# Performance work log

Measured on AMD Instinct MI355X. Metric: run time of the kernel, lower is better.

The kernel has to match this reference:

```python
import jax, jax.numpy as jnp
import numpy as np

# --- Instant-NGP hashgrid config (from INGP.build_encoding) ---
L = 16            # cfg_model.encoding.levels
F = 2             # cfg_model.encoding.hashgrid.dim
T = 1 << 19       # 2 ** log2_hashmap_size
BASE = 16         # 2 ** min_logres
FINEST = 2048     # 2 ** max_logres
GROWTH = np.exp((np.log(FINEST) - np.log(BASE)) / (L - 1))
RES = np.floor(BASE * GROWTH ** np.arange(L)).astype(np.float32)  # per-level resolution
VMIN, VMAX = -1.0, 1.0  # voxel_range
N_POINTS = 524288

# 8 trilinear corner offsets, and NGP spatial-hash primes
CORNERS = np.array([[i, j, k] for i in (0, 1) for j in (0, 1) for k in (0, 1)],
                   dtype=np.uint32)                       # [8,3]
PRIMES = np.array([1, 2654435761, 805459861], dtype=np.uint32)


def setup_inputs() -> dict:
    key = jax.random.key(0)
    k1, k2 = jax.random.split(key)
    points_3D = jax.random.uniform(k1, (N_POINTS, 3), minval=-1.0, maxval=1.0,
                                   dtype=jnp.float32)
    # torch-ngp 'uniform' init: U(-1e-4, 1e-4)
    tables = jax.random.uniform(k2, (L, T, F), minval=-1e-4, maxval=1e-4,
                                dtype=jnp.float32)
    return {"points_3D": points_3D, "tables": tables}


def _hash_encode(x, tables):
    """x: [N,3] in [0,1]; tables: [L,T,F] -> [N, L*F]."""
    corners_u = jnp.asarray(CORNERS)            # [8,3] uint32
    corners_b = jnp.asarray(CORNERS.astype(bool))
    p0u, p1u, p2u = (jnp.uint32(int(p)) for p in PRIMES)
    mask = jnp.uint32(T - 1)

    def level(table, r):
        pos = x * r                              # [N,3]
        p0 = jnp.floor(pos)
        w = pos - p0                             # trilinear weights [N,3]
        c = p0.astype(jnp.uint32)[:, None, :] + corners_u[None]  # [N,8,3]
        h = (c[..., 0] * p0u) ^ (c[..., 1] * p1u) ^ (c[..., 2] * p2u)
        idx = (h & mask).astype(jnp.int32)       # [N,8] hashed bucket ids
        vals = table[idx]                        # [N,8,F] irregular gather
        wc = jnp.where(corners_b[None], w[:, None, :], 1.0 - w[:, None, :]).prod(-1)
        return jnp.einsum('nc,ncf->nf', wc, vals)  # [N,F]

    feats = jax.vmap(level)(tables, jnp.asarray(RES))  # [L,N,F]
    n = x.shape[0]
    return jnp.transpose(feats, (1, 0, 2)).reshape(n, L * F)


def reference(points_3D, tables):
    # _encode_3D with contract=False: normalize to [0,1] over voxel_range
    x = (points_3D - VMIN) / (VMAX - VMIN)
    feat = _hash_encode(x, tables)
    return feat.astype(jnp.float32)
```

## Files before the change

kernel.cpp:

```cpp
#include <hip/hip_runtime.h>
#include <cmath>


constexpr int LVLS = 16;
constexpr unsigned TBL = 1u << 19;
constexpr unsigned TMASK = TBL - 1u;
constexpr unsigned P1 = 2654435761u;
constexpr unsigned P2 = 805459861u;
constexpr int PTS_PER_BLOCK = 512;
constexpr int NBINS = 32768;

typedef float vf2 __attribute__((ext_vector_type(2)));
typedef float vf4 __attribute__((ext_vector_type(4)));

struct ResArr { float r[LVLS]; };

__device__ __forceinline__ unsigned spread5(unsigned v) {
    v &= 31u;
    v = (v | (v << 8)) & 0x100Fu;
    v = (v | (v << 4)) & 0x10C3u;
    v = (v | (v << 2)) & 0x1249u;
    return v;
}

__device__ __forceinline__ unsigned bin_key(float px, float py, float pz) {
    float x = (px + 1.0f) * 0.5f;
    float y = (py + 1.0f) * 0.5f;
    float z = (pz + 1.0f) * 0.5f;
    unsigned bx = (unsigned)fminf(31.f, fmaxf(0.f, floorf(x * 32.f)));
    unsigned by = (unsigned)fminf(31.f, fmaxf(0.f, floorf(y * 32.f)));
    unsigned bz = (unsigned)fminf(31.f, fmaxf(0.f, floorf(z * 32.f)));
    return spread5(bx) | (spread5(by) << 1) | (spread5(bz) << 2);
}

__global__ __launch_bounds__(256) void ingp_hist(
    const float* __restrict__ pts, unsigned* __restrict__ hist, int npts)
{
    int i = blockIdx.x * 256 + threadIdx.x;
    if (i >= npts) return;
    float px = pts[i * 3 + 0], py = pts[i * 3 + 1], pz = pts[i * 3 + 2];
    atomicAdd(&hist[bin_key(px, py, pz)], 1u);
}

__global__ __launch_bounds__(1024) void ingp_scan(
    const unsigned* __restrict__ hist, unsigned* __restrict__ offs)
{
    __shared__ unsigned sc[1024];
    int t = threadIdx.x;
    unsigned loc[32];
    unsigned s = 0;
    #pragma unroll
    for (int i = 0; i < 32; ++i) { loc[i] = s; s += hist[t * 32 + i]; }
    sc[t] = s;
    __syncthreads();
    for (int d = 1; d < 1024; d <<= 1) {
        unsigned v = (t >= d) ? sc[t - d] : 0u;
        __syncthreads();
        sc[t] += v;
        __syncthreads();
    }
    unsigned base = sc[t] - s;
    #pragma unroll
    for (int i = 0; i < 32; ++i) offs[t * 32 + i] = base + loc[i];
}

__global__ __launch_bounds__(256) void ingp_scatter(
    const float* __restrict__ pts, unsigned* __restrict__ offs,
    vf4* __restrict__ pts4, int* __restrict__ perm, int npts)
{
    int i = blockIdx.x * 256 + threadIdx.x;
    if (i >= npts) return;
    float px = pts[i * 3 + 0], py = pts[i * 3 + 1], pz = pts[i * 3 + 2];
    unsigned pos = atomicAdd(&offs[bin_key(px, py, pz)], 1u);
    vf4 o; o.x = px; o.y = py; o.z = pz; o.w = __int_as_float(i);
    pts4[pos] = o;
    perm[pos] = i;
}

template<bool USE_WS, bool PACKED>
__global__ __launch_bounds__(256) void ingp_gather(
    const float* __restrict__ pts,
    const vf4* __restrict__ pts4,
    const float* __restrict__ tables,
    float2* __restrict__ dst,
    ResArr ra, int npts, int bpl)
{
    __shared__ float s_res[LVLS];
    if (threadIdx.x < LVLS) s_res[threadIdx.x] = ra.r[threadIdx.x];
    __syncthreads();

    int b = blockIdx.x;
    int lvl, q;
    if (PACKED) {
        if (b < 8 * bpl) { lvl = 8 + (b & 7); q = b >> 3; }
        else { int u = b - 8 * bpl; lvl = u / bpl; q = u - lvl * bpl; }
    } else {
        int phase_blocks = 8 * bpl;
        int xcd = b & 7;
        int phase = b / phase_blocks;
        lvl = phase == 0 ? xcd : 15 - xcd;
        q = (b % phase_blocks) >> 3;
    }
    int t = threadIdx.x;

    float r = s_res[lvl];
    const float2* __restrict__ tab = (const float2*)tables + (size_t)lvl * TBL;

    int p0 = q * PTS_PER_BLOCK + t;

    #pragma unroll
    for (int s = 0; s < 2; ++s) {
        int pglob = p0 + s * 256;
        bool valid = pglob < npts;
        int pp = valid ? pglob : 0;
        float px, py, pz;
        if (PACKED) {
            vf4 v = __builtin_nontemporal_load(pts4 + pp);
            px = v.x; py = v.y; pz = v.z;
        } else {
            px = __builtin_nontemporal_load(pts + pp * 3 + 0);
            py = __builtin_nontemporal_load(pts + pp * 3 + 1);
            pz = __builtin_nontemporal_load(pts + pp * 3 + 2);
        }
        float x = (px + 1.0f) * 0.5f;
        float y = (py + 1.0f) * 0.5f;
        float z = (pz + 1.0f) * 0.5f;
        float posx = x * r, posy = y * r, posz = z * r;
        float fx = floorf(posx), fy = floorf(posy), fz = floorf(posz);
        float wx = posx - fx, wy = posy - fy, wz = posz - fz;
        unsigned ix = (unsigned)fx, iy = (unsigned)fy, iz = (unsigned)fz;
        unsigned hx0 = ix,      hx1 = ix + 1u;
        unsigned hy0 = iy * P1;
        unsigned hz0 = iz * P2, hz1 = hz0 + P2;

        unsigned hyz[4];
        hyz[0] = hy0 ^ hz0;
        hyz[1] = hy0 ^ hz1;
        hyz[2] = (hy0 + P1) ^ hz0;
        hyz[3] = (hy0 + P1) ^ hz1;

        float2 v[8];
        if ((ix & 1u) == 0u) {
            #pragma unroll
            for (int yz = 0; yz < 4; ++yz) {
                unsigned b0 = (hx0 ^ hyz[yz]) & TMASK;
                const vf4* lp4 = (const vf4*)(tab + (b0 & ~1u));
                vf4 qd = *lp4;
                float2 lo = make_float2(qd.x, qd.y);
                float2 hi = make_float2(qd.z, qd.w);
                bool odd = (b0 & 1u) != 0u;
                v[yz]     = odd ? hi : lo;
                v[4 + yz] = odd ? lo : hi;
            }
        } else {
            #pragma unroll
            for (int yz = 0; yz < 4; ++yz) {
                unsigned b0 = (hx0 ^ hyz[yz]) & TMASK;
                unsigned b1 = (hx1 ^ hyz[yz]) & TMASK;
                v[yz]     = tab[b0];
                v[4 + yz] = tab[b1];
            }
        }

        float ox = 1.0f - wx, oy = 1.0f - wy, oz = 1.0f - wz;
        float w[8];
        w[0] = (ox * oy) * oz;
        w[1] = (ox * oy) * wz;
        w[2] = (ox * wy) * oz;
        w[3] = (ox * wy) * wz;
        w[4] = (wx * oy) * oz;
        w[5] = (wx * oy) * wz;
        w[6] = (wx * wy) * oz;
        w[7] = (wx * wy) * wz;

        float f0 = w[0] * v[0].x;
        float f1 = w[0] * v[0].y;
        #pragma unroll
        for (int c = 1; c < 8; ++c) {
            f0 += w[c] * v[c].x;
            f1 += w[c] * v[c].y;
        }
        if (valid) {
            vf2 o; o.x = f0; o.y = f1;
            if (USE_WS)
                __builtin_nontemporal_store(o, (vf2*)(dst + (size_t)lvl * npts + pglob));
            else
                dst[(size_t)pglob * LVLS + lvl] = make_float2(f0, f1);
        }
    }
}

__global__ __launch_bounds__(256) void ingp_transpose(
    const float2* __restrict__ ws, const int* __restrict__ perm,
    float4* __restrict__ out, int npts)
{
    __shared__ float2 a[LVLS][258];
    __shared__ int s_perm[256];
    int base = blockIdx.x * 256;
    int t = threadIdx.x;

    if (base + t < npts) s_perm[t] = perm ? perm[base + t] : base + t;

    #pragma unroll
    for (int l = 0; l < LVLS; ++l) {
        int pp = base + t;
        float2 val = make_float2(0.f, 0.f);
        if (pp < npts) {
            vf2 v = __builtin_nontemporal_load((const vf2*)(ws + (size_t)l * npts + pp));
            val = make_float2(v.x, v.y);
        }
        a[l][t] = val;
    }
    __syncthreads();

    int j = t & 7;
    int pl = t >> 3;
    #pragma unroll
    for (int it = 0; it < 8; ++it) {
        int pt = pl + it * 32;
        if (base + pt < npts) {
            int orig = s_perm[pt];
            float2 u = a[2 * j][pt];
            float2 v = a[2 * j + 1][pt];
            vf4 o; o.x = u.x; o.y = u.y; o.z = v.x; o.w = v.y;
            __builtin_nontemporal_store(o, (vf4*)(out + (size_t)orig * 8 + j));
        }
    }
}

extern "C" void kernel_launch(void* const* d_in, const int* in_sizes, int n_in,
                              void* d_out, int out_size, void* d_ws, size_t ws_size,
                              hipStream_t stream) {
    const float* pts    = (const float*)d_in[0];
    const float* tables = (const float*)d_in[1];
    int npts = in_sizes[0] / 3;

    ResArr ra;
    double growth = exp((log(2048.0) - log(16.0)) / 15.0);
    for (int l = 0; l < LVLS; ++l)
        ra.r[l] = (float)floor(16.0 * pow(growth, (double)l));

    int bpl = (npts + PTS_PER_BLOCK - 1) / PTS_PER_BLOCK;
    int grid = LVLS * bpl;
    int pgrid = (npts + 255) / 256;

    size_t ws_needed = (size_t)LVLS * npts * sizeof(float2);
    size_t perm_bytes = (size_t)npts * sizeof(int);
    size_t out_scratch = 2ull * NBINS * sizeof(unsigned) + (size_t)npts * sizeof(vf4);
    bool use_ws = ws_size >= ws_needed;
    bool use_sort = use_ws && (ws_size >= ws_needed + perm_bytes)
                           && ((size_t)out_size >= out_scratch);

    if (use_sort) {
        float2*   ws   = (float2*)d_ws;
        int*      perm = (int*)((char*)d_ws + ws_needed);
        unsigned* hist = (unsigned*)d_out;
        unsigned* offs = hist + NBINS;
        vf4*      pts4 = (vf4*)((char*)d_out + 2ull * NBINS * sizeof(unsigned));

        hipMemsetAsync(hist, 0, NBINS * sizeof(unsigned), stream);
        hipLaunchKernelGGL(ingp_hist, dim3(pgrid), dim3(256), 0, stream,
                           pts, hist, npts);
        hipLaunchKernelGGL(ingp_scan, dim3(1), dim3(1024), 0, stream,
                           hist, offs);
        hipLaunchKernelGGL(ingp_scatter, dim3(pgrid), dim3(256), 0, stream,
                           pts, offs, pts4, perm, npts);
        hipLaunchKernelGGL((ingp_gather<true, true>), dim3(grid), dim3(256), 0, stream,
                           nullptr, pts4, tables, ws, ra, npts, bpl);
        hipLaunchKernelGGL(ingp_transpose, dim3(pgrid), dim3(256), 0, stream,
                           ws, perm, (float4*)d_out, npts);
    } else if (use_ws) {
        float2* ws = (float2*)d_ws;
        hipLaunchKernelGGL((ingp_gather<true, false>), dim3(grid), dim3(256), 0, stream,
                           pts, nullptr, tables, ws, ra, npts, bpl);
        hipLaunchKernelGGL(ingp_transpose, dim3(pgrid), dim3(256), 0, stream,
                           ws, (const int*)nullptr, (float4*)d_out, npts);
    } else {
        hipLaunchKernelGGL((ingp_gather<false, false>), dim3(grid), dim3(256), 0, stream,
                           pts, nullptr, tables, (float2*)d_out, ra, npts, bpl);
    }
}
```

Before: 334.7 us.

## Fuse per-level gather and transpose into one per-point kernel over all levels

Replaces the level-major gather kernel plus transpose/permutation kernel with a single kernel where each thread loops over all 16 levels and writes its full feature row to the output using the original index stored in the sorted points. This removes the intermediate workspace round trip, the perm array and one launch. In exchange, all hash tables are accessed concurrently by each block, losing the per-level L2/XCD locality, and register pressure rises from holding 32 accumulators.

Result: slower. 449.7 us (+34.3%).

```diff
diff --git a/kernel.cpp b/kernel.cpp
--- a/kernel.cpp
+++ b/kernel.cpp
@@ -7,7 +7,6 @@
 constexpr unsigned TMASK = TBL - 1u;
 constexpr unsigned P1 = 2654435761u;
 constexpr unsigned P2 = 805459861u;
-constexpr int PTS_PER_BLOCK = 512;
 constexpr int NBINS = 32768;
 
 typedef float vf2 __attribute__((ext_vector_type(2)));
@@ -66,7 +65,7 @@
 
 __global__ __launch_bounds__(256) void ingp_scatter(
     const float* __restrict__ pts, unsigned* __restrict__ offs,
-    vf4* __restrict__ pts4, int* __restrict__ perm, int npts)
+    vf4* __restrict__ pts4, int npts)
 {
     int i = blockIdx.x * 256 + threadIdx.x;
     if (i >= npts) return;
@@ -74,57 +73,40 @@
     unsigned pos = atomicAdd(&offs[bin_key(px, py, pz)], 1u);
     vf4 o; o.x = px; o.y = py; o.z = pz; o.w = __int_as_float(i);
     pts4[pos] = o;
-    perm[pos] = i;
-}
-
-template<bool USE_WS, bool PACKED>
-__global__ __launch_bounds__(256) void ingp_gather(
+}
+
+template<bool SORTED>
+__global__ __launch_bounds__(256) void ingp_fused(
     const float* __restrict__ pts,
     const vf4* __restrict__ pts4,
     const float* __restrict__ tables,
-    float2* __restrict__ dst,
-    ResArr ra, int npts, int bpl)
-{
-    __shared__ float s_res[LVLS];
-    if (threadIdx.x < LVLS) s_res[threadIdx.x] = ra.r[threadIdx.x];
-    __syncthreads();
-
-    int b = blockIdx.x;
-    int lvl, q;
-    if (PACKED) {
-        if (b < 8 * bpl) { lvl = 8 + (b & 7); q = b >> 3; }
-        else { int u = b - 8 * bpl; lvl = u / bpl; q = u - lvl * bpl; }
+    vf4* __restrict__ out,
+    ResArr ra, int npts)
+{
+    int i = blockIdx.x * 256 + threadIdx.x;
+    bool valid = i < npts;
+    int pp = valid ? i : 0;
+    float px, py, pz; int orig;
+    if (SORTED) {
+        vf4 v = __builtin_nontemporal_load(pts4 + pp);
+        px = v.x; py = v.y; pz = v.z; orig = __float_as_int(v.w);
     } else {
-        int phase_blocks = 8 * bpl;
-        int xcd = b & 7;
-        int phase = b / phase_blocks;
-        lvl = phase == 0 ? xcd : 15 - xcd;
-        q = (b % phase_blocks) >> 3;
-    }
-    int t = threadIdx.x;
-
-    float r = s_res[lvl];
-    const float2* __restrict__ tab = (const float2*)tables + (size_t)lvl * TBL;
-
-    int p0 = q * PTS_PER_BLOCK + t;
+        px = pts[pp * 3 + 0];
+        py = pts[pp * 3 + 1];
+        pz = pts[pp * 3 + 2];
+        orig = pp;
+    }
+    float x = (px + 1.0f) * 0.5f;
+    float y = (py + 1.0f) * 0.5f;
+    float z = (pz + 1.0f) * 0.5f;
+
+    float acc[2 * LVLS];
 
     #pragma unroll
-    for (int s = 0; s < 2; ++s) {
-        int pglob = p0 + s * 256;
-        bool valid = pglob < npts;
-        int pp = valid ? pglob : 0;
-        float px, py, pz;
-        if (PACKED) {
-            vf4 v = __builtin_nontemporal_load(pts4 + pp);
-            px = v.x; py = v.y; pz = v.z;
-        } else {
-            px = __builtin_nontemporal_load(pts + pp * 3 + 0);
-            py = __builtin_nontemporal_load(pts + pp * 3 + 1);
-            pz = __builtin_nontemporal_load(pts + pp * 3 + 2);
-        }
-        float x = (px + 1.0f) * 0.5f;
-        float y = (py + 1.0f) * 0.5f;
-        float z = (pz + 1.0f) * 0.5f;
+    for (int l = 0; l < LVLS; ++l) {
+        float r = ra.r[l];
+        const float2* __restrict__ tab = (const float2*)tables + (size_t)l * TBL;
+
         float posx = x * r, posy = y * r, posz = z * r;
         float fx = floorf(posx), fy = floorf(posy), fz = floorf(posz);
         float wx = posx - fx, wy = posy - fy, wz = posz - fz;
@@ -180,50 +162,18 @@
             f0 += w[c] * v[c].x;
             f1 += w[c] * v[c].y;
         }
-        if (valid) {
-            vf2 o; o.x = f0; o.y = f1;
-            if (USE_WS)
-                __builtin_nontemporal_store(o, (vf2*)(dst + (size_t)lvl * npts + pglob));
-            else
-                dst[(size_t)pglob * LVLS + lvl] = make_float2(f0, f1);
-        }
-    }
-}
-
-__global__ __launch_bounds__(256) void ingp_transpose(
-    const float2* __restrict__ ws, const int* __restrict__ perm,
-    float4* __restrict__ out, int npts)
-{
-    __shared__ float2 a[LVLS][258];
-    __shared__ int s_perm[256];
-    int base = blockIdx.x * 256;
-    int t = threadIdx.x;
-
-    if (base + t < npts) s_perm[t] = perm ? perm[base + t] : base + t;
-
-    #pragma unroll
-    for (int l = 0; l < LVLS; ++l) {
-        int pp = base + t;
-        float2 val = make_float2(0.f, 0.f);
-        if (pp < npts) {
-            vf2 v = __builtin_nontemporal_load((const vf2*)(ws + (size_t)l * npts + pp));
-            val = make_float2(v.x, v.y);
-        }
-        a[l][t] = val;
-    }
-    __syncthreads();
-
-    int j = t & 7;
-    int pl = t >> 3;
-    #pragma unroll
-    for (int it = 0; it < 8; ++it) {
-        int pt = pl + it * 32;
-        if (base + pt < npts) {
-            int orig = s_perm[pt];
-            float2 u = a[2 * j][pt];
-            float2 v = a[2 * j + 1][pt];
-            vf4 o; o.x = u.x; o.y = u.y; o.z = v.x; o.w = v.y;
-            __builtin_nontemporal_store(o, (vf4*)(out + (size_t)orig * 8 + j));
+        acc[2 * l]     = f0;
+        acc[2 * l + 1] = f1;
+    }
+
+    if (valid) {
+        vf4* row = out + (size_t)orig * 8;
+        #pragma unroll
+        for (int k = 0; k < 8; ++k) {
+            vf4 o;
+            o.x = acc[4 * k + 0]; o.y = acc[4 * k + 1];
+            o.z = acc[4 * k + 2]; o.w = acc[4 * k + 3];
+            __builtin_nontemporal_store(o, row + k);
         }
     }
 }
@@ -240,23 +190,15 @@
     for (int l = 0; l < LVLS; ++l)
         ra.r[l] = (float)floor(16.0 * pow(growth, (double)l));
 
-    int bpl = (npts + PTS_PER_BLOCK - 1) / PTS_PER_BLOCK;
-    int grid = LVLS * bpl;
     int pgrid = (npts + 255) / 256;
 
-    size_t ws_needed = (size_t)LVLS * npts * sizeof(float2);
-    size_t perm_bytes = (size_t)npts * sizeof(int);
-    size_t out_scratch = 2ull * NBINS * sizeof(unsigned) + (size_t)npts * sizeof(vf4);
-    bool use_ws = ws_size >= ws_needed;
-    bool use_sort = use_ws && (ws_size >= ws_needed + perm_bytes)
-                           && ((size_t)out_size >= out_scratch);
+    size_t sort_bytes = 2ull * NBINS * sizeof(unsigned) + (size_t)npts * sizeof(vf4);
+    bool use_sort = ws_size >= sort_bytes;
 
     if (use_sort) {
-        float2*   ws   = (float2*)d_ws;
-        int*      perm = (int*)((char*)d_ws + ws_needed);
-        unsigned* hist = (unsigned*)d_out;
+        unsigned* hist = (unsigned*)d_ws;
         unsigned* offs = hist + NBINS;
-        vf4*      pts4 = (vf4*)((char*)d_out + 2ull * NBINS * sizeof(unsigned));
+        vf4*      pts4 = (vf4*)((char*)d_ws + 2ull * NBINS * sizeof(unsigned));
 
         hipMemsetAsync(hist, 0, NBINS * sizeof(unsigned), stream);
         hipLaunchKernelGGL(ingp_hist, dim3(pgrid), dim3(256), 0, stream,
@@ -264,19 +206,11 @@
         hipLaunchKernelGGL(ingp_scan, dim3(1), dim3(1024), 0, stream,
                            hist, offs);
         hipLaunchKernelGGL(ingp_scatter, dim3(pgrid), dim3(256), 0, stream,
-                           pts, offs, pts4, perm, npts);
-        hipLaunchKernelGGL((ingp_gather<true, true>), dim3(grid), dim3(256), 0, stream,
-                           nullptr, pts4, tables, ws, ra, npts, bpl);
-        hipLaunchKernelGGL(ingp_transpose, dim3(pgrid), dim3(256), 0, stream,
-                           ws, perm, (float4*)d_out, npts);
-    } else if (use_ws) {
-        float2* ws = (float2*)d_ws;
-        hipLaunchKernelGGL((ingp_gather<true, false>), dim3(grid), dim3(256), 0, stream,
-                           pts, nullptr, tables, ws, ra, npts, bpl);
-        hipLaunchKernelGGL(ingp_transpose, dim3(pgrid), dim3(256), 0, stream,
-                           ws, (const int*)nullptr, (float4*)d_out, npts);
+                           pts, offs, pts4, npts);
+        hipLaunchKernelGGL((ingp_fused<true>), dim3(pgrid), dim3(256), 0, stream,
+                           nullptr, pts4, tables, (vf4*)d_out, ra, npts);
     } else {
-        hipLaunchKernelGGL((ingp_gather<false, false>), dim3(grid), dim3(256), 0, stream,
-                           pts, nullptr, tables, (float2*)d_out, ra, npts, bpl);
-    }
-}
+        hipLaunchKernelGGL((ingp_fused<false>), dim3(pgrid), dim3(256), 0, stream,
+                           pts, nullptr, tables, (vf4*)d_out, ra, npts);
+    }
+}
```
